# Performance work log

Hardware: AMD Instinct MI355X
Metric: run time of the kernel (lower is better)

The kernel has to match this reference:

```python
import jax, jax.numpy as jnp
import numpy as np

N_NODES = 20000
N_EDGES = 240000
IN_DIM = 20
SH_DIM = 16  # (lmax+1)^2 with lmax=3
DENOM = 1.0
EPS = 1e-12


def spherical_harmonics_lmax3(v):
    """Real spherical harmonics l=0..3 on unit vectors v: [E,3] -> [E,16]."""
    x, y, z = v[:, 0], v[:, 1], v[:, 2]
    x2, y2, z2 = x * x, y * y, z * z
    sh = [
        jnp.full_like(x, 0.28209479177387814),            # l=0
        0.4886025119029199 * y,                            # l=1, m=-1
        0.4886025119029199 * z,                            # l=1, m=0
        0.4886025119029199 * x,                            # l=1, m=1
        1.0925484305920792 * x * y,                        # l=2, m=-2
        1.0925484305920792 * y * z,                        # l=2, m=-1
        0.31539156525252005 * (3.0 * z2 - 1.0),            # l=2, m=0
        1.0925484305920792 * x * z,                        # l=2, m=1
        0.5462742152960396 * (x2 - y2),                    # l=2, m=2
        0.5900435899266435 * y * (3.0 * x2 - y2),          # l=3, m=-3
        2.890611442640554 * x * y * z,                     # l=3, m=-2
        0.4570457994644658 * y * (5.0 * z2 - 1.0),         # l=3, m=-1
        0.3731763325901154 * z * (5.0 * z2 - 3.0),         # l=3, m=0
        0.4570457994644658 * x * (5.0 * z2 - 1.0),         # l=3, m=1
        1.445305721320277 * z * (x2 - y2),                 # l=3, m=2
        0.5900435899266435 * x * (x2 - 3.0 * y2),          # l=3, m=3
    ]
    return jnp.stack(sh, axis=-1)


def setup_inputs() -> dict:
    key = jax.random.key(0)
    ks = jax.random.split(key, 10)
    x = jax.random.normal(ks[0], (N_NODES, IN_DIM), dtype=jnp.float32)
    positions = jax.random.normal(ks[1], (N_NODES, 3), dtype=jnp.float32)
    edge_index = jax.random.randint(ks[2], (2, N_EDGES), 0, N_NODES, dtype=jnp.int32)
    s = 1.0 / np.sqrt(IN_DIM)
    W_pre = jax.random.uniform(ks[3], (IN_DIM, IN_DIM), jnp.float32, -s, s)
    b_pre = jax.random.uniform(ks[4], (IN_DIM,), jnp.float32, -s, s)
    W_post = jax.random.uniform(ks[5], (IN_DIM, IN_DIM), jnp.float32, -s, s)
    b_post = jax.random.uniform(ks[6], (IN_DIM,), jnp.float32, -s, s)
    W_sc = jax.random.uniform(ks[7], (IN_DIM, IN_DIM), jnp.float32, -s, s)
    b_sc = jax.random.uniform(ks[8], (IN_DIM,), jnp.float32, -s, s)
    return {"x": x, "positions": positions, "edge_index": edge_index,
            "W_pre": W_pre, "b_pre": b_pre, "W_post": W_post, "b_post": b_post,
            "W_sc": W_sc, "b_sc": b_sc}


def reference(x, positions, edge_index, W_pre, b_pre, W_post, b_post, W_sc, b_sc):
    row, col = edge_index[0], edge_index[1]
    # per-edge gather + relative positions
    rel = positions[col] - positions[row]                      # [E,3]
    norm = jnp.sqrt(jnp.sum(rel * rel, axis=-1, keepdims=True) + EPS)
    sh = spherical_harmonics_lmax3(rel / norm)                 # [E,16]
    sender = x[row]                                            # [E,20]
    # equivariant tensor product (outer product over irreps channels)
    tp = (sender[:, :, None] * sh[:, None, :]).reshape(sender.shape[0], IN_DIM * SH_DIM)  # [E,320]
    edge_features = jnp.concatenate([sender, tp], axis=1)      # [E,340]
    # scatter-add aggregation to target nodes
    aggr = jax.ops.segment_sum(edge_features, col, num_segments=N_NODES)  # [N,340]
    # node update MLP + shortcut (math of Layer.update)
    h = x / DENOM
    h = jax.nn.relu(h @ W_pre.T + b_pre)
    h = h @ W_post.T + b_post
    out = x @ W_sc.T + b_sc + h                                # [N,20]
    # aggr is computed (and aggregated) by the original propagate; concat so it stays live
    return jnp.concatenate([out, aggr], axis=1)                # [N,360]
```

## Files before the change

kernel.cpp:

```cpp
#include <hip/hip_runtime.h>
#include <stdint.h>

#define N_NODES 20000
#define N_EDGES 240000
#define IN_DIM  20
#define OUT_DIM 360
#define EPS_F   1e-12f
#define CAP     64
#define EDGE_BLOCKS ((N_EDGES + 255) / 256)
#define MLP_BLOCKS  ((N_NODES + 255) / 256)

typedef _Float16 half8   __attribute__((ext_vector_type(8)));
typedef float    floatx16 __attribute__((ext_vector_type(16)));

__device__ __forceinline__ half8 h8_from_u32(uint32_t u0, uint32_t u1,
                                             uint32_t u2, uint32_t u3) {
    union { uint32_t u[4]; half8 h; } t;
    t.u[0] = u0; t.u[1] = u1; t.u[2] = u2; t.u[3] = u3;
    return t.h;
}

__device__ __forceinline__ uint32_t maskpair(int t, int j) {
    return (t > j ? 0xFFFFu : 0u) | (t > j + 1 ? 0xFFFF0000u : 0u);
}

__device__ float sh_coeff(int k, float xn, float yn, float zn) {
    const float x2 = xn * xn, y2 = yn * yn, z2 = zn * zn;
    switch (k) {
        case 0:  return 0.28209479177387814f;
        case 1:  return 0.4886025119029199f * yn;
        case 2:  return 0.4886025119029199f * zn;
        case 3:  return 0.4886025119029199f * xn;
        case 4:  return 1.0925484305920792f * xn * yn;
        case 5:  return 1.0925484305920792f * yn * zn;
        case 6:  return 0.31539156525252005f * (3.0f * z2 - 1.0f);
        case 7:  return 1.0925484305920792f * xn * zn;
        case 8:  return 0.5462742152960396f * (x2 - y2);
        case 9:  return 0.5900435899266435f * yn * (3.0f * x2 - y2);
        case 10: return 2.890611442640554f  * xn * yn * zn;
        case 11: return 0.4570457994644658f * yn * (5.0f * z2 - 1.0f);
        case 12: return 0.3731763325901154f * zn * (5.0f * z2 - 3.0f);
        case 13: return 0.4570457994644658f * xn * (5.0f * z2 - 1.0f);
        case 14: return 1.445305721320277f  * zn * (x2 - y2);
        default: return 0.5900435899266435f * xn * (x2 - 3.0f * y2);
    }
}

__device__ __noinline__ floatx16 ovf_accum(floatx16 acc, int node, int col, int hi,
    const float* __restrict__ x, const float* __restrict__ pos,
    const int* __restrict__ ei, const int* __restrict__ ovf_cnt,
    const int* __restrict__ ovf)
{
    const int mm = *ovf_cnt;
    for (int t2 = 0; t2 < mm; ++t2) {
        const int e = ovf[t2];
        if (ei[N_EDGES + e] != node) continue;
        const int row = ei[e];
        const float rx = pos[node * 3 + 0] - pos[row * 3 + 0];
        const float ry = pos[node * 3 + 1] - pos[row * 3 + 1];
        const float rz = pos[node * 3 + 2] - pos[row * 3 + 2];
        const float rinv = rsqrtf(rx * rx + ry * ry + rz * rz + EPS_F);
        float shc;
        if (col < 16)       shc = sh_coeff(col, rx * rinv, ry * rinv, rz * rinv);
        else if (col == 16) shc = 1.0f;
        else                shc = 0.0f;
#pragma unroll
        for (int r = 0; r < 16; ++r) {
            const int rw = ((r & 3) + 8 * (r >> 2)) + 4 * hi;
            if (rw < IN_DIM)
                acc[r] = fmaf(x[(size_t)row * IN_DIM + rw], shc, acc[r]);
        }
    }
    return acc;
}

__global__ __launch_bounds__(256) void bucket_mlp(
    const int* __restrict__ ei,
    const float* __restrict__ x,
    const float* __restrict__ Wpre,  const float* __restrict__ bpre,
    const float* __restrict__ Wpost, const float* __restrict__ bpost,
    const float* __restrict__ Wsc,   const float* __restrict__ bsc,
    int* __restrict__ counts,
    int* __restrict__ ovf_cnt,
    int* __restrict__ ovf,
    uint16_t* __restrict__ bucket16,
    uint32_t* __restrict__ xpair,
    float* __restrict__ out)
{
    if ((int)blockIdx.x < EDGE_BLOCKS) {
        const int e = (int)(blockIdx.x * 256 + threadIdx.x);
        if (e >= N_EDGES) return;
        const int row = ei[e];
        const int col = ei[N_EDGES + e];
        const int slot = atomicAdd(&counts[col], 1);
        if (slot >= CAP) { ovf[atomicAdd(ovf_cnt, 1)] = e; return; }
        bucket16[col * CAP + slot] = (uint16_t)row;
        return;
    }

    __shared__ float smw[1260];
    for (int t = (int)threadIdx.x; t < 400; t += 256) {
        smw[t]       = Wpre[t];
        smw[400 + t] = Wpost[t];
        smw[800 + t] = Wsc[t];
    }
    if (threadIdx.x < IN_DIM) {
        smw[1200 + threadIdx.x]              = bpre[threadIdx.x];
        smw[1200 + IN_DIM + threadIdx.x]     = bpost[threadIdx.x];
        smw[1200 + 2 * IN_DIM + threadIdx.x] = bsc[threadIdx.x];
    }
    __syncthreads();

    const int i = (int)((blockIdx.x - EDGE_BLOCKS) * 256 + threadIdx.x);
    if (i >= N_NODES) return;

    const float* sWpre  = smw;
    const float* sWpost = smw + 400;
    const float* sWsc   = smw + 800;
    const float* sb     = smw + 1200;

    float xi[IN_DIM], h[IN_DIM];
#pragma unroll
    for (int j = 0; j < IN_DIM; ++j) xi[j] = x[(size_t)i * IN_DIM + j];

#pragma unroll
    for (int j = 0; j < IN_DIM; ++j) {
        const float v = xi[j];
        const _Float16 hh = (_Float16)v;
        const float res = v - (float)hh;
        union { _Float16 f[2]; uint32_t u; } t;
        t.f[0] = hh; t.f[1] = (_Float16)res;
        xpair[(size_t)i * IN_DIM + j] = t.u;
    }

#pragma unroll
    for (int j = 0; j < IN_DIM; ++j) {
        float a = sb[j];
#pragma unroll
        for (int kk = 0; kk < IN_DIM; ++kk) a = fmaf(xi[kk], sWpre[j * IN_DIM + kk], a);
        h[j] = fmaxf(a, 0.0f);
    }
#pragma unroll
    for (int j = 0; j < IN_DIM; ++j) {
        float a = sb[IN_DIM + j] + sb[2 * IN_DIM + j];
#pragma unroll
        for (int kk = 0; kk < IN_DIM; ++kk) {
            a = fmaf(h[kk],  sWpost[j * IN_DIM + kk], a);
            a = fmaf(xi[kk], sWsc[j * IN_DIM + kk],  a);
        }
        out[(size_t)i * OUT_DIM + j] = a;
    }
}

__global__ __launch_bounds__(256) void node_gather(
    const float* __restrict__ x,
    const float* __restrict__ pos,
    const int* __restrict__ ei,
    const int* __restrict__ counts,
    const uint16_t* __restrict__ bucket16,
    const uint32_t* __restrict__ xpair,
    const int* __restrict__ ovf_cnt,
    const int* __restrict__ ovf,
    float* __restrict__ out)
{
    __shared__ uint16_t shls[4][64][16];

    const int lane  = (int)(threadIdx.x & 63);
    const int w     = (int)(threadIdx.x >> 6);
    const int node  = __builtin_amdgcn_readfirstlane(
        (int)((blockIdx.x * blockDim.x + threadIdx.x) >> 6));
    const int col   = lane & 31;
    const int hi    = lane >> 5;
    const int khalf = hi * 8;
    const int rowc  = min(col, IN_DIM - 1);

    const int cnt_raw = __builtin_amdgcn_readfirstlane(counts[node]);
    const int cnt = min(cnt_raw, CAP);

    int rl = 0;
    if (lane < cnt) {
        rl = (int)bucket16[node * CAP + lane];
        const float rx = pos[node * 3 + 0] - pos[rl * 3 + 0];
        const float ry = pos[node * 3 + 1] - pos[rl * 3 + 1];
        const float rz = pos[node * 3 + 2] - pos[rl * 3 + 2];
        const float rinv = rsqrtf(rx * rx + ry * ry + rz * rz + EPS_F);
        const float xx = rx * rinv, yy = ry * rinv, zz = rz * rinv;
        const float x2 = xx * xx, y2 = yy * yy, z2 = zz * zz;

        const float sh0  = 0.28209479177387814f;
        const float sh1  = 0.4886025119029199f * yy;
        const float sh2  = 0.4886025119029199f * zz;
        const float sh3  = 0.4886025119029199f * xx;
        const float sh4  = 1.0925484305920792f * xx * yy;
        const float sh5  = 1.0925484305920792f * yy * zz;
        const float sh6  = 0.31539156525252005f * (3.0f * z2 - 1.0f);
        const float sh7  = 1.0925484305920792f * xx * zz;
        const float sh8  = 0.5462742152960396f * (x2 - y2);
        const float sh9  = 0.5900435899266435f * yy * (3.0f * x2 - y2);
        const float sh10 = 2.890611442640554f  * xx * yy * zz;
        const float sh11 = 0.4570457994644658f * yy * (5.0f * z2 - 1.0f);
        const float sh12 = 0.3731763325901154f * zz * (5.0f * z2 - 3.0f);
        const float sh13 = 0.4570457994644658f * xx * (5.0f * z2 - 1.0f);
        const float sh14 = 1.445305721320277f  * zz * (x2 - y2);
        const float sh15 = 0.5900435899266435f * xx * (x2 - 3.0f * y2);

        const half8 v0 = { (_Float16)sh0,  (_Float16)sh1,  (_Float16)sh2,  (_Float16)sh3,
                           (_Float16)sh4,  (_Float16)sh5,  (_Float16)sh6,  (_Float16)sh7 };
        const half8 v1 = { (_Float16)sh8,  (_Float16)sh9,  (_Float16)sh10, (_Float16)sh11,
                           (_Float16)sh12, (_Float16)sh13, (_Float16)sh14, (_Float16)sh15 };
        half8* wp = (half8*)&shls[w][lane][0];
        wp[0] = v0;
        wp[1] = v1;
    }

    floatx16 acc = {0,0,0,0,0,0,0,0,0,0,0,0,0,0,0,0};

    if (cnt > 0) {
        const int nb = (cnt + 15) >> 4;
        for (int b = 0; b < nb; ++b) {
            const int sbase = 16 * b + khalf;

            int rr[8];
#pragma unroll
            for (int j = 0; j < 8; ++j)
                rr[j] = __shfl(rl, sbase + j, 64);

            uint32_t ee[8];
#pragma unroll
            for (int j = 0; j < 8; ++j)
                ee[j] = (sbase + j < cnt && col < IN_DIM)
                      ? xpair[(size_t)rr[j] * IN_DIM + rowc] : 0u;

            uint32_t B0, B1, B2, B3;
            if (col < 16) {
                const uint32_t h0 = shls[w][sbase + 0][col];
                const uint32_t h1 = shls[w][sbase + 1][col];
                const uint32_t h2 = shls[w][sbase + 2][col];
                const uint32_t h3 = shls[w][sbase + 3][col];
                const uint32_t h4 = shls[w][sbase + 4][col];
                const uint32_t h5 = shls[w][sbase + 5][col];
                const uint32_t h6 = shls[w][sbase + 6][col];
                const uint32_t h7 = shls[w][sbase + 7][col];
                B0 = h0 | (h1 << 16);
                B1 = h2 | (h3 << 16);
                B2 = h4 | (h5 << 16);
                B3 = h6 | (h7 << 16);
            } else if (col == 16) {
                B0 = B1 = B2 = B3 = 0x3C003C00u;
            } else {
                B0 = B1 = B2 = B3 = 0u;
            }
            const int rem = cnt - 16 * b;
            if (rem < 16) {
                const int t = rem - khalf;
                B0 &= maskpair(t, 0);
                B1 &= maskpair(t, 2);
                B2 &= maskpair(t, 4);
                B3 &= maskpair(t, 6);
            }

            uint32_t a1u[4], a2u[4];
#pragma unroll
            for (int pq = 0; pq < 4; ++pq) {
                a1u[pq] = (ee[2 * pq] & 0xFFFFu)  | (ee[2 * pq + 1] << 16);
                a2u[pq] = (ee[2 * pq] >> 16)      | (ee[2 * pq + 1] & 0xFFFF0000u);
            }

            const half8 hb  = h8_from_u32(B0, B1, B2, B3);
            const half8 ha1 = h8_from_u32(a1u[0], a1u[1], a1u[2], a1u[3]);
            const half8 ha2 = h8_from_u32(a2u[0], a2u[1], a2u[2], a2u[3]);
            acc = __builtin_amdgcn_mfma_f32_32x32x16_f16(ha1, hb, acc, 0, 0, 0);
            acc = __builtin_amdgcn_mfma_f32_32x32x16_f16(ha2, hb, acc, 0, 0, 0);
        }
    }

    if (cnt_raw > CAP)
        acc = ovf_accum(acc, node, col, hi, x, pos, ei, ovf_cnt, ovf);

    float* orow = out + (size_t)node * OUT_DIM;
    if (col < 16) {
#pragma unroll
        for (int r = 0; r < 16; ++r) {
            const int rw = ((r & 3) + 8 * (r >> 2)) + 4 * hi;
            if (rw < IN_DIM) orow[2 * IN_DIM + rw * 16 + col] = acc[r];
        }
    } else if (col == 16) {
#pragma unroll
        for (int r = 0; r < 16; ++r) {
            const int rw = ((r & 3) + 8 * (r >> 2)) + 4 * hi;
            if (rw < IN_DIM) orow[IN_DIM + rw] = acc[r];
        }
    }
}

extern "C" void kernel_launch(void* const* d_in, const int* in_sizes, int n_in,
                              void* d_out, int out_size, void* d_ws, size_t ws_size,
                              hipStream_t stream)
{
    const float* x     = (const float*)d_in[0];
    const float* pos   = (const float*)d_in[1];
    const int*   ei    = (const int*)d_in[2];
    const float* Wpre  = (const float*)d_in[3];
    const float* bpre  = (const float*)d_in[4];
    const float* Wpost = (const float*)d_in[5];
    const float* bpost = (const float*)d_in[6];
    const float* Wsc   = (const float*)d_in[7];
    const float* bsc   = (const float*)d_in[8];
    float* out = (float*)d_out;

    char* wp = (char*)d_ws;
    uint16_t* bucket16 = (uint16_t*)wp;   wp += (size_t)N_NODES * CAP * 2;
    uint32_t* xpair    = (uint32_t*)wp;   wp += (size_t)N_NODES * IN_DIM * 4;
    int*      counts   = (int*)wp;        wp += (size_t)N_NODES * 4;
    int*      ovf_cnt  = (int*)wp;        wp += 4;
    int*      ovf      = (int*)wp;

    hipMemsetAsync(counts, 0, (size_t)(N_NODES + 1) * sizeof(int), stream);

    bucket_mlp<<<EDGE_BLOCKS + MLP_BLOCKS, 256, 0, stream>>>(
        ei, x, Wpre, bpre, Wpost, bpost, Wsc, bsc,
        counts, ovf_cnt, ovf, bucket16, xpair, out);

    node_gather<<<(N_NODES * 64) / 256, 256, 0, stream>>>(
        x, pos, ei, counts, bucket16, xpair, ovf_cnt, ovf, out);
}
```

Before: 118.2 us.

## Split per-node edge counters into eight cache-line-padded partitions

Result: no change. 116.5 us (-1.4%).

```diff
diff --git a/kernel.cpp b/kernel.cpp
--- a/kernel.cpp
+++ b/kernel.cpp
@@ -6,7 +6,9 @@
 #define IN_DIM  20
 #define OUT_DIM 360
 #define EPS_F   1e-12f
-#define CAP     64
+#define NPART   8
+#define CAP_P   16
+#define SLOTS   (NPART * CAP_P)
 #define EDGE_BLOCKS ((N_EDGES + 255) / 256)
 #define MLP_BLOCKS  ((N_NODES + 255) / 256)
 
@@ -80,7 +82,7 @@
     const float* __restrict__ Wpre,  const float* __restrict__ bpre,
     const float* __restrict__ Wpost, const float* __restrict__ bpost,
     const float* __restrict__ Wsc,   const float* __restrict__ bsc,
-    int* __restrict__ counts,
+    int* __restrict__ cnt_pad,
     int* __restrict__ ovf_cnt,
     int* __restrict__ ovf,
     uint16_t* __restrict__ bucket16,
@@ -90,11 +92,12 @@
     if ((int)blockIdx.x < EDGE_BLOCKS) {
         const int e = (int)(blockIdx.x * 256 + threadIdx.x);
         if (e >= N_EDGES) return;
+        const int p = (int)(blockIdx.x & (NPART - 1));
         const int row = ei[e];
         const int col = ei[N_EDGES + e];
-        const int slot = atomicAdd(&counts[col], 1);
-        if (slot >= CAP) { ovf[atomicAdd(ovf_cnt, 1)] = e; return; }
-        bucket16[col * CAP + slot] = (uint16_t)row;
+        const int slot = atomicAdd(&cnt_pad[((size_t)(p * N_NODES + col)) << 4], 1);
+        if (slot >= CAP_P) { ovf[atomicAdd(ovf_cnt, 1)] = e; return; }
+        bucket16[col * SLOTS + (p << 4) + slot] = (uint16_t)row;
         return;
     }
 
@@ -156,7 +159,7 @@
     const float* __restrict__ x,
     const float* __restrict__ pos,
     const int* __restrict__ ei,
-    const int* __restrict__ counts,
+    const int* __restrict__ cnt_pad,
     const uint16_t* __restrict__ bucket16,
     const uint32_t* __restrict__ xpair,
     const int* __restrict__ ovf_cnt,
@@ -174,12 +177,32 @@
     const int khalf = hi * 8;
     const int rowc  = min(col, IN_DIM - 1);
 
-    const int cnt_raw = __builtin_amdgcn_readfirstlane(counts[node]);
-    const int cnt = min(cnt_raw, CAP);
+    int ovf_any = 0;
+    int c[NPART];
+#pragma unroll
+    for (int q = 0; q < NPART; ++q) {
+        const int cr = __builtin_amdgcn_readfirstlane(
+            cnt_pad[((size_t)(q * N_NODES + node)) << 4]);
+        ovf_any |= (cr > CAP_P);
+        c[q] = min(cr, CAP_P);
+    }
+    int pre = 0, pp = 0, base = 0;
+#pragma unroll
+    for (int q = 0; q < NPART; ++q) {
+        if (q >= 1) {
+            const int ge = (lane >= pre) ? 1 : 0;
+            pp  += ge;
+            base = ge ? pre : base;
+        }
+        pre += c[q];
+    }
+    const int cnt = min(pre, 64);
+    const int s  = min(lane - base, CAP_P - 1);
+    const int m  = (pp << 4) + s;
 
     int rl = 0;
     if (lane < cnt) {
-        rl = (int)bucket16[node * CAP + lane];
+        rl = (int)bucket16[node * SLOTS + m];
         const float rx = pos[node * 3 + 0] - pos[rl * 3 + 0];
         const float ry = pos[node * 3 + 1] - pos[rl * 3 + 1];
         const float rz = pos[node * 3 + 2] - pos[rl * 3 + 2];
@@ -274,7 +297,7 @@
         }
     }
 
-    if (cnt_raw > CAP)
+    if (ovf_any)
         acc = ovf_accum(acc, node, col, hi, x, pos, ei, ovf_cnt, ovf);
 
     float* orow = out + (size_t)node * OUT_DIM;
@@ -309,18 +332,18 @@
     float* out = (float*)d_out;
 
     char* wp = (char*)d_ws;
-    uint16_t* bucket16 = (uint16_t*)wp;   wp += (size_t)N_NODES * CAP * 2;
+    uint16_t* bucket16 = (uint16_t*)wp;   wp += (size_t)N_NODES * SLOTS * 2;
     uint32_t* xpair    = (uint32_t*)wp;   wp += (size_t)N_NODES * IN_DIM * 4;
-    int*      counts   = (int*)wp;        wp += (size_t)N_NODES * 4;
+    int*      cnt_pad  = (int*)wp;        wp += (size_t)NPART * N_NODES * 64;
     int*      ovf_cnt  = (int*)wp;        wp += 4;
     int*      ovf      = (int*)wp;
 
-    hipMemsetAsync(counts, 0, (size_t)(N_NODES + 1) * sizeof(int), stream);
+    hipMemsetAsync(cnt_pad, 0, (size_t)NPART * N_NODES * 64 + 4, stream);
 
     bucket_mlp<<<EDGE_BLOCKS + MLP_BLOCKS, 256, 0, stream>>>(
         ei, x, Wpre, bpre, Wpost, bpost, Wsc, bsc,
-        counts, ovf_cnt, ovf, bucket16, xpair, out);
+        cnt_pad, ovf_cnt, ovf, bucket16, xpair, out);
 
     node_gather<<<(N_NODES * 64) / 256, 256, 0, stream>>>(
-        x, pos, ei, counts, bucket16, xpair, ovf_cnt, ovf, out);
-}
+        x, pos, ei, cnt_pad, bucket16, xpair, ovf_cnt, ovf, out);
+}
```
